# Kernel tuning notes

Hardware: AMD Instinct MI355X
Metric: run time of the kernel (lower is better)

The kernel has to match this reference:

```python
import jax, jax.numpy as jnp
import numpy as np

BATCH, N_IN, N_OUT, D = 32768, 256, 256, 8

def setup_inputs() -> dict:
    key = jax.random.key(0)
    k1, k2 = jax.random.split(key)
    noise_std = 1.0 / (N_IN * (D + 1))
    x = jax.random.normal(k1, (BATCH, N_IN), dtype=jnp.float32)
    c_basis = noise_std * jax.random.normal(k2, (N_OUT, N_IN, D + 1), dtype=jnp.float32)
    c_act = jnp.ones((N_OUT, N_IN), dtype=jnp.float32)
    return {"x": x, "c_basis": c_basis, "c_act": c_act}

def _cheby_basis(x, degree):
    # x: (batch, n_in) -> (batch, n_in, degree+1) Chebyshev T_k(tanh(x))
    t = jnp.tanh(x)
    polys = [jnp.ones_like(t), t]
    for _ in range(2, degree + 1):
        polys.append(2.0 * t * polys[-1] - polys[-2])
    return jnp.stack(polys[: degree + 1], axis=-1)

def reference(x, c_basis, c_act):
    batch = x.shape[0]
    n_out = c_basis.shape[0]
    degree = c_basis.shape[-1] - 1
    Ti = _cheby_basis(x, degree)                      # (batch, n_in, D+1)
    cheb = Ti.reshape(batch, -1)                      # (batch, n_in*(D+1))
    cheb_w = (c_basis * c_act[..., None]).reshape(n_out, -1)
    return jnp.matmul(cheb, cheb_w.T)                 # (batch, n_out)
```

## Files before the change

kernel.cpp:

```cpp
#include <hip/hip_runtime.h>
#include <hip/hip_bf16.h>

#define BATCH 32768
#define NIN   256
#define NOUT  256

typedef __attribute__((ext_vector_type(8))) short bf16x8;
typedef __attribute__((ext_vector_type(4))) float f32x4;
typedef __attribute__((ext_vector_type(2))) float f32x2;
typedef __attribute__((ext_vector_type(4))) unsigned int u32x4;

static __device__ __forceinline__ unsigned short bf16_rne(float f) {
  unsigned u = __float_as_uint(f);
  u += 0x7fffu + ((u >> 16) & 1u);
  return (unsigned short)(u >> 16);
}

static __device__ __forceinline__ float fast_tanh(float v) {
  float a = fabsf(v);
  float z = __expf(-2.0f * a);
  float r = (1.0f - z) * __builtin_amdgcn_rcpf(1.0f + z);
  return copysignf(r, v);
}

static __device__ __forceinline__ unsigned pack_pair(f32x2 v) {
  __hip_bfloat162 h2 = __float22bfloat162_rn(make_float2(v[0], v[1]));
  union { __hip_bfloat162 h; unsigned u; } cv;
  cv.h = h2;
  return cv.u;
}

static __device__ __forceinline__ void init_state(const f32x4 x0, const f32x4 x1,
                                                  f32x2* cur, f32x2* prev,
                                                  f32x2* t2) {
  #pragma unroll
  for (int p = 0; p < 4; ++p) {
    float va = (p < 2) ? x0[2 * p]     : x1[2 * p - 4];
    float vb = (p < 2) ? x0[2 * p + 1] : x1[2 * p - 3];
    float ta = fast_tanh(va);
    float tb = fast_tanh(vb);
    cur[p]  = (f32x2){ta, tb};
    t2[p]   = cur[p] + cur[p];
    prev[p] = (f32x2){1.0f, 1.0f};
  }
}

static __device__ __forceinline__ void phase_barrier() {
  __builtin_amdgcn_sched_barrier(0);
  __builtin_amdgcn_s_barrier();
  __builtin_amdgcn_sched_barrier(0);
}

__global__ void cheby_prep(const float* __restrict__ cb,
                           const float* __restrict__ ca,
                           unsigned short* __restrict__ Bp,
                           float* __restrict__ bias) {
  __shared__ float red[256];
  int n = blockIdx.x;
  int i = threadIdx.x;

  const float* cp = cb + ((size_t)n * NIN + i) * 9;
  f32x4 c0 = *(const f32x4*)cp;
  f32x4 c1 = *(const f32x4*)(cp + 4);
  float c8  = cp[8];
  float av  = ca[(size_t)n * NIN + i];

  int ic   = i >> 5;
  int kg   = (i >> 3) & 3;
  int j    = i & 7;
  int tile = n >> 4;
  int col  = n & 15;
  size_t base = (size_t)kg * 128 + col * 8 + j;
  #pragma unroll
  for (int dm = 0; dm < 8; ++dm) {
    float w = ((dm < 3) ? c0[dm + 1] : (dm < 7) ? c1[dm - 3] : c8) * av;
    Bp[(((size_t)dm * 8 + ic) * 16 + tile) * 512 + base] = bf16_rne(w);
  }

  red[i] = c0[0] * av;
  __syncthreads();
  #pragma unroll
  for (int s = 128; s >= 64; s >>= 1) {
    if (i < s) red[i] += red[i + s];
    __syncthreads();
  }
  if (i < 64) {
    float v = red[i];
    #pragma unroll
    for (int off = 32; off; off >>= 1) v += __shfl_down(v, off);
    if (i == 0) bias[n] = v;
  }
}

__global__ __launch_bounds__(512, 2)
void cheby_mfma(const float* __restrict__ x,
                const unsigned short* __restrict__ Bp,
                const float* __restrict__ bias,
                float* __restrict__ out) {
  __shared__ unsigned short Asm_[2][8][8][512];

  int tid  = threadIdx.x;
  int w    = tid >> 6;
  int lane = tid & 63;
  int row16 = lane & 15;
  int kg    = lane >> 4;

  int wr = w >> 2;
  int wc = w & 3;
  int base_row = blockIdx.x * 128;
  int tile0    = wc * 4;

  const float* xw = x + (size_t)(base_row + w * 16 + row16) * NIN + kg * 8;
  char* wbase = (char*)Asm_ + (w * 1024 + lane * 16);
  const char* abase   = (const char*)Asm_ + lane * 16;
  const char* bp_lane = (const char*)Bp + kg * 256 + row16 * 16;

  f32x4 acc[4][4];
  #pragma unroll
  for (int a = 0; a < 4; ++a)
    #pragma unroll
    for (int b = 0; b < 4; ++b) acc[a][b] = (f32x4)0.0f;

  f32x4 xa = *(const f32x4*)xw;
  f32x4 xb = *(const f32x4*)(xw + 4);
  {
    f32x2 c0[4], p0[4], t0[4];
    init_state(xa, xb, c0, p0, t0);
    #pragma unroll
    for (int d = 1; d <= 8; ++d) {
      u32x4 pk;
      #pragma unroll
      for (int q = 0; q < 4; ++q) pk[q] = pack_pair(c0[q]);
      *(u32x4*)(wbase + (d - 1) * 8192) = pk;
      if (d < 8) {
        #pragma unroll
        for (int q = 0; q < 4; ++q) {
          f32x2 nx = __builtin_elementwise_fma(t0[q], c0[q], -p0[q]);
          p0[q] = c0[q];
          c0[q] = nx;
        }
      }
    }
  }
  xa = *(const f32x4*)(xw + 32);
  xb = *(const f32x4*)(xw + 36);
  f32x2 cur[4], prev[4], t2[4];
  init_state(xa, xb, cur, prev, t2);

  bf16x8 af[2][4], bfr[2][4];
  {
    const char* bp0 = bp_lane + (size_t)tile0 * 1024;
    #pragma unroll
    for (int nt = 0; nt < 4; ++nt)
      bfr[0][nt] = *(const bf16x8*)(bp0 + nt * 1024);
  }
  __builtin_amdgcn_sched_barrier(0);
  asm volatile("s_waitcnt lgkmcnt(0)" ::: "memory");
  __builtin_amdgcn_s_barrier();
  __builtin_amdgcn_sched_barrier(0);
  #pragma unroll
  for (int mt = 0; mt < 4; ++mt)
    af[0][mt] = *(const bf16x8*)(abase + (wr * 4 + mt) * 1024);

  for (int ic = 0; ic < 7; ++ic) {
    const char* ai   = abase + (ic & 1) * 65536 + (wr * 4) * 1024;
    const char* ain  = abase + ((ic + 1) & 1) * 65536 + (wr * 4) * 1024;
    char*       wp   = wbase + ((ic + 1) & 1) * 65536;
    const char* bpi  = bp_lane + (size_t)(ic * 16 + tile0) * 1024;
    const char* bpin = bp_lane + (size_t)((ic + 1) * 16 + tile0) * 1024;

    #pragma unroll
    for (int p = 0; p < 8; ++p) {
      if (p < 7) {
        #pragma unroll
        for (int mt = 0; mt < 4; ++mt)
          af[(p + 1) & 1][mt] =
              *(const bf16x8*)(ai + (p + 1) * 8192 + mt * 1024);
      } else {
        #pragma unroll
        for (int mt = 0; mt < 4; ++mt)
          af[0][mt] = *(const bf16x8*)(ain + mt * 1024);
      }
      if (p < 7) {
        #pragma unroll
        for (int nt = 0; nt < 4; ++nt)
          bfr[(p + 1) & 1][nt] =
              *(const bf16x8*)(bpi + (size_t)(p + 1) * 131072 + nt * 1024);
      } else {
        #pragma unroll
        for (int nt = 0; nt < 4; ++nt)
          bfr[0][nt] = *(const bf16x8*)(bpin + nt * 1024);
      }
      {
        u32x4 pk;
        #pragma unroll
        for (int q = 0; q < 4; ++q) pk[q] = pack_pair(cur[q]);
        *(u32x4*)(wp + p * 8192) = pk;
        if (p < 7) {
          #pragma unroll
          for (int q = 0; q < 4; ++q) {
            f32x2 nx = __builtin_elementwise_fma(t2[q], cur[q], -prev[q]);
            prev[q] = cur[q];
            cur[q]  = nx;
          }
        }
      }
      if (p == 3 && ic <= 5) {
        xa = *(const f32x4*)(xw + (ic + 2) * 32);
        xb = *(const f32x4*)(xw + (ic + 2) * 32 + 4);
      }
      if (p == 7 && ic <= 5)
        init_state(xa, xb, cur, prev, t2);

      phase_barrier();

      __builtin_amdgcn_s_setprio(1);
      #pragma unroll
      for (int mt = 0; mt < 4; ++mt)
        #pragma unroll
        for (int nt = 0; nt < 4; ++nt)
          acc[mt][nt] = __builtin_amdgcn_mfma_f32_16x16x32_bf16(
              af[p & 1][mt], bfr[p & 1][nt], acc[mt][nt], 0, 0, 0);
      __builtin_amdgcn_s_setprio(0);
    }
  }

  {
    const char* ai  = abase + 65536 + (wr * 4) * 1024;
    const char* bpi = bp_lane + (size_t)(7 * 16 + tile0) * 1024;
    #pragma unroll
    for (int p = 0; p < 8; ++p) {
      if (p < 7) {
        #pragma unroll
        for (int mt = 0; mt < 4; ++mt)
          af[(p + 1) & 1][mt] =
              *(const bf16x8*)(ai + (p + 1) * 8192 + mt * 1024);
        #pragma unroll
        for (int nt = 0; nt < 4; ++nt)
          bfr[(p + 1) & 1][nt] =
              *(const bf16x8*)(bpi + (size_t)(p + 1) * 131072 + nt * 1024);
      }
      __builtin_amdgcn_s_setprio(1);
      #pragma unroll
      for (int mt = 0; mt < 4; ++mt)
        #pragma unroll
        for (int nt = 0; nt < 4; ++nt)
          acc[mt][nt] = __builtin_amdgcn_mfma_f32_16x16x32_bf16(
              af[p & 1][mt], bfr[p & 1][nt], acc[mt][nt], 0, 0, 0);
      __builtin_amdgcn_s_setprio(0);
    }
  }

  #pragma unroll
  for (int nt = 0; nt < 4; ++nt) {
    int c = (tile0 + nt) * 16 + row16;
    float bv = bias[c];
    #pragma unroll
    for (int mt = 0; mt < 4; ++mt) {
      int r0 = base_row + wr * 64 + mt * 16 + kg * 4;
      #pragma unroll
      for (int q = 0; q < 4; ++q)
        out[(size_t)(r0 + q) * NOUT + c] = acc[mt][nt][q] + bv;
    }
  }
}

extern "C" void kernel_launch(void* const* d_in, const int* in_sizes, int n_in,
                              void* d_out, int out_size, void* d_ws, size_t ws_size,
                              hipStream_t stream) {
  const float* x  = (const float*)d_in[0];
  const float* cb = (const float*)d_in[1];
  const float* ca = (const float*)d_in[2];
  float* out = (float*)d_out;

  unsigned short* Bp = (unsigned short*)d_ws;
  float* bias = (float*)((char*)d_ws + 8 * NIN * NOUT * 2);

  cheby_prep<<<NOUT, 256, 0, stream>>>(cb, ca, Bp, bias);
  cheby_mfma<<<256, 512, 0, stream>>>(x, Bp, bias, out);
}
```

Before: 45.51 us.

## Ping-pong wave roles alternating MFMA windows with prefetch and basis generation

Restructures the main loop so even and odd waves take opposite roles in each barrier window. One group runs a pair of MFMA k-slices while the other prefetches the next pair of A/B fragments and computes the Chebyshev slices, then they swap. The goal is to stop MFMA from stalling behind LDS and VALU work by keeping the matrix unit fed from one wave group at a time. This uses more fragment registers (two k-slices buffered), and the lgkmcnt wait inside every barrier could serialize memory latency.

```diff
diff --git a/kernel.cpp b/kernel.cpp
--- a/kernel.cpp
+++ b/kernel.cpp
@@ -45,8 +45,9 @@
   }
 }
 
-static __device__ __forceinline__ void phase_barrier() {
+static __device__ __forceinline__ void window_barrier() {
   __builtin_amdgcn_sched_barrier(0);
+  asm volatile("s_waitcnt lgkmcnt(0)" ::: "memory");
   __builtin_amdgcn_s_barrier();
   __builtin_amdgcn_sched_barrier(0);
 }
@@ -109,6 +110,7 @@
   int wc = w & 3;
   int base_row = blockIdx.x * 128;
   int tile0    = wc * 4;
+  const bool role0 = ((w & 1) == 0);
 
   const float* xw = x + (size_t)(base_row + w * 16 + row16) * NIN + kg * 8;
   char* wbase = (char*)Asm_ + (w * 1024 + lane * 16);
@@ -127,12 +129,12 @@
     f32x2 c0[4], p0[4], t0[4];
     init_state(xa, xb, c0, p0, t0);
     #pragma unroll
-    for (int d = 1; d <= 8; ++d) {
+    for (int d = 0; d < 8; ++d) {
       u32x4 pk;
       #pragma unroll
       for (int q = 0; q < 4; ++q) pk[q] = pack_pair(c0[q]);
-      *(u32x4*)(wbase + (d - 1) * 8192) = pk;
-      if (d < 8) {
+      *(u32x4*)(wbase + d * 8192) = pk;
+      if (d < 7) {
         #pragma unroll
         for (int q = 0; q < 4; ++q) {
           f32x2 nx = __builtin_elementwise_fma(t0[q], c0[q], -p0[q]);
@@ -147,22 +149,69 @@
   f32x2 cur[4], prev[4], t2[4];
   init_state(xa, xb, cur, prev, t2);
 
-  bf16x8 af[2][4], bfr[2][4];
-  {
-    const char* bp0 = bp_lane + (size_t)tile0 * 1024;
-    #pragma unroll
-    for (int nt = 0; nt < 4; ++nt)
-      bfr[0][nt] = *(const bf16x8*)(bp0 + nt * 1024);
-  }
-  __builtin_amdgcn_sched_barrier(0);
-  asm volatile("s_waitcnt lgkmcnt(0)" ::: "memory");
-  __builtin_amdgcn_s_barrier();
-  __builtin_amdgcn_sched_barrier(0);
-  #pragma unroll
-  for (int mt = 0; mt < 4; ++mt)
-    af[0][mt] = *(const bf16x8*)(abase + (wr * 4 + mt) * 1024);
-
-  for (int ic = 0; ic < 7; ++ic) {
+  window_barrier();
+
+  bf16x8 af2[2][4], bf2[2][4];
+  if (role0) {
+    const char* a0 = abase + (wr * 4) * 1024;
+    const char* b0 = bp_lane + (size_t)tile0 * 1024;
+    #pragma unroll
+    for (int dd = 0; dd < 2; ++dd) {
+      #pragma unroll
+      for (int mt = 0; mt < 4; ++mt)
+        af2[dd][mt] = *(const bf16x8*)(a0 + dd * 8192 + mt * 1024);
+      #pragma unroll
+      for (int nt = 0; nt < 4; ++nt)
+        bf2[dd][nt] = *(const bf16x8*)(b0 + (size_t)dd * 131072 + nt * 1024);
+    }
+  }
+
+#define MFMA_PAIR()                                                      \
+    __builtin_amdgcn_s_setprio(1);                                       \
+    _Pragma("unroll")                                                    \
+    for (int dd = 0; dd < 2; ++dd)                                       \
+      _Pragma("unroll")                                                  \
+      for (int mt = 0; mt < 4; ++mt)                                     \
+        _Pragma("unroll")                                                \
+        for (int nt = 0; nt < 4; ++nt)                                   \
+          acc[mt][nt] = __builtin_amdgcn_mfma_f32_16x16x32_bf16(         \
+              af2[dd][mt], bf2[dd][nt], acc[mt][nt], 0, 0, 0);           \
+    __builtin_amdgcn_s_setprio(0)
+
+#define PREFETCH_PAIR(ABASE, BBASE, D0)                                  \
+    _Pragma("unroll")                                                    \
+    for (int dd = 0; dd < 2; ++dd) {                                     \
+      _Pragma("unroll")                                                  \
+      for (int mt = 0; mt < 4; ++mt)                                     \
+        af2[dd][mt] =                                                    \
+            *(const bf16x8*)((ABASE) + ((D0) + dd) * 8192 + mt * 1024);  \
+      _Pragma("unroll")                                                  \
+      for (int nt = 0; nt < 4; ++nt)                                     \
+        bf2[dd][nt] = *(const bf16x8*)((BBASE) +                         \
+            (size_t)((D0) + dd) * 131072 + nt * 1024);                   \
+    }
+
+#define SLICES(Q)                                                        \
+    if (ic < 7) {                                                        \
+      _Pragma("unroll")                                                  \
+      for (int s2 = 0; s2 < 2; ++s2) {                                   \
+        u32x4 pk;                                                        \
+        _Pragma("unroll")                                                \
+        for (int q = 0; q < 4; ++q) pk[q] = pack_pair(cur[q]);           \
+        *(u32x4*)(wp + (2 * (Q) + s2) * 8192) = pk;                      \
+        if (2 * (Q) + s2 < 7) {                                          \
+          _Pragma("unroll")                                              \
+          for (int q = 0; q < 4; ++q) {                                  \
+            f32x2 nx =                                                   \
+                __builtin_elementwise_fma(t2[q], cur[q], -prev[q]);      \
+            prev[q] = cur[q];                                            \
+            cur[q]  = nx;                                                \
+          }                                                              \
+        }                                                                \
+      }                                                                  \
+    }
+
+  for (int ic = 0; ic < 8; ++ic) {
     const char* ai   = abase + (ic & 1) * 65536 + (wr * 4) * 1024;
     const char* ain  = abase + ((ic + 1) & 1) * 65536 + (wr * 4) * 1024;
     char*       wp   = wbase + ((ic + 1) & 1) * 65536;
@@ -170,86 +219,39 @@
     const char* bpin = bp_lane + (size_t)((ic + 1) * 16 + tile0) * 1024;
 
     #pragma unroll
-    for (int p = 0; p < 8; ++p) {
-      if (p < 7) {
-        #pragma unroll
-        for (int mt = 0; mt < 4; ++mt)
-          af[(p + 1) & 1][mt] =
-              *(const bf16x8*)(ai + (p + 1) * 8192 + mt * 1024);
+    for (int l = 0; l < 8; ++l) {
+      if (role0) {
+        if ((l & 1) == 0) {
+          MFMA_PAIR();
+        } else {
+          if (l < 7) {
+            PREFETCH_PAIR(ai, bpi, l + 1);
+          } else if (ic < 7) {
+            PREFETCH_PAIR(ain, bpin, 0);
+          }
+          SLICES(l >> 1);
+        }
       } else {
-        #pragma unroll
-        for (int mt = 0; mt < 4; ++mt)
-          af[0][mt] = *(const bf16x8*)(ain + mt * 1024);
-      }
-      if (p < 7) {
-        #pragma unroll
-        for (int nt = 0; nt < 4; ++nt)
-          bfr[(p + 1) & 1][nt] =
-              *(const bf16x8*)(bpi + (size_t)(p + 1) * 131072 + nt * 1024);
-      } else {
-        #pragma unroll
-        for (int nt = 0; nt < 4; ++nt)
-          bfr[0][nt] = *(const bf16x8*)(bpin + nt * 1024);
-      }
-      {
-        u32x4 pk;
-        #pragma unroll
-        for (int q = 0; q < 4; ++q) pk[q] = pack_pair(cur[q]);
-        *(u32x4*)(wp + p * 8192) = pk;
-        if (p < 7) {
-          #pragma unroll
-          for (int q = 0; q < 4; ++q) {
-            f32x2 nx = __builtin_elementwise_fma(t2[q], cur[q], -prev[q]);
-            prev[q] = cur[q];
-            cur[q]  = nx;
-          }
+        if ((l & 1) == 0) {
+          PREFETCH_PAIR(ai, bpi, l);
+          SLICES(l >> 1);
+        } else {
+          MFMA_PAIR();
         }
       }
-      if (p == 3 && ic <= 5) {
+      if (l == 3 && ic <= 5) {
         xa = *(const f32x4*)(xw + (ic + 2) * 32);
         xb = *(const f32x4*)(xw + (ic + 2) * 32 + 4);
       }
-      if (p == 7 && ic <= 5)
+      if (l == 7 && ic <= 5)
         init_state(xa, xb, cur, prev, t2);
 
-      phase_barrier();
-
-      __builtin_amdgcn_s_setprio(1);
-      #pragma unroll
-      for (int mt = 0; mt < 4; ++mt)
-        #pragma unroll
-        for (int nt = 0; nt < 4; ++nt)
-          acc[mt][nt] = __builtin_amdgcn_mfma_f32_16x16x32_bf16(
-              af[p & 1][mt], bfr[p & 1][nt], acc[mt][nt], 0, 0, 0);
-      __builtin_amdgcn_s_setprio(0);
-    }
-  }
-
-  {
-    const char* ai  = abase + 65536 + (wr * 4) * 1024;
-    const char* bpi = bp_lane + (size_t)(7 * 16 + tile0) * 1024;
-    #pragma unroll
-    for (int p = 0; p < 8; ++p) {
-      if (p < 7) {
-        #pragma unroll
-        for (int mt = 0; mt < 4; ++mt)
-          af[(p + 1) & 1][mt] =
-              *(const bf16x8*)(ai + (p + 1) * 8192 + mt * 1024);
-        #pragma unroll
-        for (int nt = 0; nt < 4; ++nt)
-          bfr[(p + 1) & 1][nt] =
-              *(const bf16x8*)(bpi + (size_t)(p + 1) * 131072 + nt * 1024);
-      }
-      __builtin_amdgcn_s_setprio(1);
-      #pragma unroll
-      for (int mt = 0; mt < 4; ++mt)
-        #pragma unroll
-        for (int nt = 0; nt < 4; ++nt)
-          acc[mt][nt] = __builtin_amdgcn_mfma_f32_16x16x32_bf16(
-              af[p & 1][mt], bfr[p & 1][nt], acc[mt][nt], 0, 0, 0);
-      __builtin_amdgcn_s_setprio(0);
-    }
-  }
+      if (!(ic == 7 && l == 7)) window_barrier();
+    }
+  }
+#undef SLICES
+#undef PREFETCH_PAIR
+#undef MFMA_PAIR
 
   #pragma unroll
   for (int nt = 0; nt < 4; ++nt) {
```

Result: slower. 52.95 us (+16.3%).
